# Optimization experiments

Hardware: AMD Instinct MI355X
Metric: run time of the kernel (lower is better)

The kernel has to match this reference:

```python
import jax, jax.numpy as jnp
import numpy as np

T, A, H, E = 16, 8, 128, 32  # steps, actions/step, hidden, embed


def setup_inputs() -> dict:
    key = jax.random.key(0)
    ks = jax.random.split(key, 16)
    n = lambda k, s: jax.random.normal(k, s, dtype=jnp.float32) * 0.1
    return {
        "old_actions": jax.random.randint(ks[0], (T,), 0, A),
        "init_input": n(ks[1], (1, E)),
        "W_ih_a": n(ks[2], (4 * H, E)), "W_hh_a": n(ks[3], (4 * H, H)),
        "b_ih_a": n(ks[4], (4 * H,)), "b_hh_a": n(ks[5], (4 * H,)),
        "heads_W": n(ks[6], (T, A, H)), "heads_b": n(ks[7], (T, A)),
        "W_ih_c": n(ks[8], (4 * H, E)), "W_hh_c": n(ks[9], (4 * H, H)),
        "b_ih_c": n(ks[10], (4 * H,)), "b_hh_c": n(ks[11], (4 * H,)),
        "critic_W": n(ks[12], (1, H)), "critic_b": n(ks[13], (1,)),
        "embed": n(ks[14], (T * A, E)),
    }


def _lstm_cell(x, h, c, W_ih, W_hh, b_ih, b_hh):
    # PyTorch LSTMCell: gate order i, f, g, o
    g = W_ih @ x + b_ih + W_hh @ h + b_hh
    i, f, gg, o = jnp.split(g, 4)
    c = jax.nn.sigmoid(f) * c + jax.nn.sigmoid(i) * jnp.tanh(gg)
    h = jax.nn.sigmoid(o) * jnp.tanh(c)
    return h, c


def reference(old_actions, init_input, W_ih_a, W_hh_a, b_ih_a, b_hh_a,
              heads_W, heads_b, W_ih_c, W_hh_c, b_ih_c, b_hh_c,
              critic_W, critic_b, embed):
    # input sequence is fully determined by the given actions
    global_idx = jnp.arange(T) * A + old_actions          # action offsets
    emb_rows = embed[global_idx]                          # [T, E]
    x_seq = jnp.concatenate([init_input, emb_rows[:-1]], axis=0)  # [T, E]

    def step(carry, xs):
        h_a, c_a, h_c, c_c = carry
        x, hw, hb, a = xs
        h_a, c_a = _lstm_cell(x, h_a, c_a, W_ih_a, W_hh_a, b_ih_a, b_hh_a)
        logits = hw @ h_a + hb                            # [A]
        logp = jax.nn.log_softmax(logits)
        probs = jnp.exp(logp)
        lp = logp[a]
        ent = -jnp.sum(probs * logp)
        h_c, c_c = _lstm_cell(x, h_c, c_c, W_ih_c, W_hh_c, b_ih_c, b_hh_c)
        val = critic_W[0] @ h_c + critic_b[0]
        return (h_a, c_a, h_c, c_c), (lp, ent, val)

    z = jnp.zeros((H,), jnp.float32)
    _, (log_probs, entropies, values) = jax.lax.scan(
        step, (z, z, z, z), (x_seq, heads_W, heads_b, old_actions))
    return log_probs, entropies, values  # each [T]
```

## Files before the change

### kernel.cpp

```cpp
#include <hip/hip_runtime.h>
#include <math.h>

#define T 16
#define A 8
#define H 128
#define E 32
#define G (4*H)

#define WS_WHH(L)   ((size_t)(L) * 131072u)
#define WS_ACCX(L)  (262144u + (size_t)(L) * 16384u)

typedef _Float16 h2t __attribute__((ext_vector_type(2)));
typedef _Float16 h8t __attribute__((ext_vector_type(8)));

__device__ __forceinline__ float sigmoidf_(float x) {
    return 1.0f / (1.0f + __expf(-x));
}
__device__ __forceinline__ float tanhf_(float x) {
    return 1.0f - 2.0f / (1.0f + __expf(2.0f * x));
}

#if __has_builtin(__builtin_amdgcn_fdot2)
#define DOT2(a, b, c) __builtin_amdgcn_fdot2((a), (b), (c), false)
#else
__device__ __forceinline__ float dot2_fb(h2t a, h2t b, float c) {
    return fmaf((float)a[0], (float)b[0], fmaf((float)a[1], (float)b[1], c));
}
#define DOT2(a, b, c) dot2_fb((a), (b), (c))
#endif

#define RPT16(M) M(0) M(1) M(2) M(3) M(4) M(5) M(6) M(7) \
                 M(8) M(9) M(10) M(11) M(12) M(13) M(14) M(15)

__global__ __launch_bounds__(256)
void ppo_prep_kernel(const int* __restrict__ old_actions,
                     const float* __restrict__ init_input,
                     const float* __restrict__ W_ih_a, const float* __restrict__ W_hh_a,
                     const float* __restrict__ b_ih_a, const float* __restrict__ b_hh_a,
                     const float* __restrict__ W_ih_c, const float* __restrict__ W_hh_c,
                     const float* __restrict__ b_ih_c, const float* __restrict__ b_hh_c,
                     const float* __restrict__ embed,
                     char* __restrict__ ws)
{
    const int b = blockIdx.x;
    if (b < 64) {
        int tau  = b * 256 + threadIdx.x;
        int lstm = tau >> 13;
        int i    = tau & 8191;
        int r    = i >> 4;
        int c    = i & 15;
        const float* W = (lstm == 0) ? W_hh_a : W_hh_c;
        const float* src = W + r * H + c * 8;
        float4 fa = *(const float4*)(src);
        float4 fb = *(const float4*)(src + 4);
        h8t p = { (_Float16)fa.x, (_Float16)fa.y, (_Float16)fa.z, (_Float16)fa.w,
                  (_Float16)fb.x, (_Float16)fb.y, (_Float16)fb.z, (_Float16)fb.w };
        *(h8t*)(ws + WS_WHH(lstm) + (size_t)(c * 512 + r) * 16u) = p;
    } else {
        int tau  = (b - 64) * 256 + threadIdx.x;
        int lstm = tau >> 13;
        int i    = tau & 8191;
        int t    = i >> 9;
        int r    = i & 511;
        const float* W_ih = (lstm == 0) ? W_ih_a : W_ih_c;
        const float* b_ih = (lstm == 0) ? b_ih_a : b_ih_c;
        const float* b_hh = (lstm == 0) ? b_hh_a : b_hh_c;
        const float* xp = (t == 0) ? init_input
                                   : embed + ((t - 1) * A + old_actions[t - 1]) * E;
        const float* wr = W_ih + r * E;
        float s0 = 0.f, s1 = 0.f, s2 = 0.f, s3 = 0.f;
        #pragma unroll
        for (int e = 0; e < E; e += 4) {
            float4 wv = *(const float4*)(wr + e);
            float4 xv = *(const float4*)(xp + e);
            s0 = fmaf(wv.x, xv.x, s0); s1 = fmaf(wv.y, xv.y, s1);
            s2 = fmaf(wv.z, xv.z, s2); s3 = fmaf(wv.w, xv.w, s3);
        }
        float acc = b_ih[r] + b_hh[r] + ((s0 + s1) + (s2 + s3));
        *(_Float16*)(ws + WS_ACCX(lstm) + (size_t)(t * 512 + r) * 2u) = (_Float16)acc;
    }
}

__global__ __attribute__((amdgpu_flat_work_group_size(512, 512),
                          amdgpu_waves_per_eu(2, 2)))
void ppo_ctrl_kernel(const int* __restrict__ old_actions,
                     const float* __restrict__ heads_W, const float* __restrict__ heads_b,
                     const float* __restrict__ critic_W, const float* __restrict__ critic_b,
                     const char* __restrict__ ws,
                     float* __restrict__ out)
{
    const int tid  = threadIdx.x;
    const int lane = tid & 63;
    const int wv   = tid >> 6;
    const int lstm = blockIdx.x;
    const bool actor = (lstm == 0);

    __shared__ __align__(16) float gates_s[G];
    __shared__ __align__(16) _Float16 h16[H];
    __shared__ __align__(16) _Float16 hhist[T][H];

    const char* wbase = ws + WS_WHH(lstm);
#define LOADW(i) h8t w##i = *(const h8t*)(wbase + (size_t)((i) * 512 + tid) * 16u); \
        asm volatile("" : "+v"(w##i));
    RPT16(LOADW)
#undef LOADW

    const _Float16* accg = (const _Float16*)(ws + WS_ACCX(lstm));

    float c_reg = 0.0f;
    const h8t* hv = (const h8t*)h16;

    #pragma unroll 1
    for (int t = 0; t < T; ++t) {
        float axv = (float)accg[t * 512 + tid];
        float a0 = 0.f, a1 = 0.f, a2 = 0.f, a3 = 0.f;
        if (t != 0) {
#define MACC(i) { h8t hq = hv[i];                                          \
            a0 = DOT2(__builtin_shufflevector(w##i, w##i, 0, 1),           \
                      __builtin_shufflevector(hq,  hq,  0, 1), a0);        \
            a1 = DOT2(__builtin_shufflevector(w##i, w##i, 2, 3),           \
                      __builtin_shufflevector(hq,  hq,  2, 3), a1);        \
            a2 = DOT2(__builtin_shufflevector(w##i, w##i, 4, 5),           \
                      __builtin_shufflevector(hq,  hq,  4, 5), a2);        \
            a3 = DOT2(__builtin_shufflevector(w##i, w##i, 6, 7),           \
                      __builtin_shufflevector(hq,  hq,  6, 7), a3); }
            RPT16(MACC)
#undef MACC
        }
        gates_s[tid] = axv + ((a0 + a1) + (a2 + a3));
        __syncthreads();

        if (tid < H) {
            float gi = gates_s[tid],       gf = gates_s[tid + H];
            float gg = gates_s[tid + 2*H], go = gates_s[tid + 3*H];
            float cn = sigmoidf_(gf) * c_reg + sigmoidf_(gi) * tanhf_(gg);
            c_reg = cn;
            float hvv = sigmoidf_(go) * tanhf_(cn);
            _Float16 hf = (_Float16)hvv;
            h16[tid] = hf;
            hhist[t][tid] = hf;
        }
        __syncthreads();
    }

    if (actor) {
        #pragma unroll
        for (int rep = 0; rep < 2; ++rep) {
            const int tt = wv + rep * 8;
            float hA = (float)hhist[tt][lane];
            float hB = (float)hhist[tt][64 + lane];
#define LOGIT(a) float l##a; {                                            \
            const float* hw = heads_W + (tt * A + (a)) * H;               \
            float p = fmaf(hw[lane], hA, hw[64 + lane] * hB);             \
            p += __shfl_xor(p, 1);  p += __shfl_xor(p, 2);                \
            p += __shfl_xor(p, 4);  p += __shfl_xor(p, 8);                \
            p += __shfl_xor(p, 16); p += __shfl_xor(p, 32);               \
            l##a = p + heads_b[tt * A + (a)]; }
            LOGIT(0) LOGIT(1) LOGIT(2) LOGIT(3)
            LOGIT(4) LOGIT(5) LOGIT(6) LOGIT(7)
#undef LOGIT
            if (lane == 0) {
                float m = fmaxf(fmaxf(fmaxf(l0, l1), fmaxf(l2, l3)),
                                fmaxf(fmaxf(l4, l5), fmaxf(l6, l7)));
                float e0 = __expf(l0 - m), e1 = __expf(l1 - m),
                      e2 = __expf(l2 - m), e3 = __expf(l3 - m),
                      e4 = __expf(l4 - m), e5 = __expf(l5 - m),
                      e6 = __expf(l6 - m), e7 = __expf(l7 - m);
                float s = ((e0 + e1) + (e2 + e3)) + ((e4 + e5) + (e6 + e7));
                float logZ = m + __logf(s);
                int act = old_actions[tt];
                float la = (act == 0) ? l0 : (act == 1) ? l1 : (act == 2) ? l2 :
                           (act == 3) ? l3 : (act == 4) ? l4 : (act == 5) ? l5 :
                           (act == 6) ? l6 : l7;
                out[tt] = la - logZ;
                float w_ = e0*(l0-logZ) + e1*(l1-logZ) + e2*(l2-logZ) + e3*(l3-logZ)
                         + e4*(l4-logZ) + e5*(l5-logZ) + e6*(l6-logZ) + e7*(l7-logZ);
                out[T + tt] = -w_ / s;
            }
        }
    } else {
        #pragma unroll
        for (int rep = 0; rep < 2; ++rep) {
            const int tt = wv + rep * 8;
            float hA = (float)hhist[tt][lane];
            float hB = (float)hhist[tt][64 + lane];
            float p = fmaf(critic_W[lane], hA, critic_W[64 + lane] * hB);
            p += __shfl_xor(p, 1);  p += __shfl_xor(p, 2);
            p += __shfl_xor(p, 4);  p += __shfl_xor(p, 8);
            p += __shfl_xor(p, 16); p += __shfl_xor(p, 32);
            if (lane == 0) out[2 * T + tt] = p + critic_b[0];
        }
    }
}

extern "C" void kernel_launch(void* const* d_in, const int* in_sizes, int n_in,
                              void* d_out, int out_size, void* d_ws, size_t ws_size,
                              hipStream_t stream) {
    const int*   old_actions = (const int*)  d_in[0];
    const float* init_input  = (const float*)d_in[1];
    const float* W_ih_a      = (const float*)d_in[2];
    const float* W_hh_a      = (const float*)d_in[3];
    const float* b_ih_a      = (const float*)d_in[4];
    const float* b_hh_a      = (const float*)d_in[5];
    const float* heads_W     = (const float*)d_in[6];
    const float* heads_b     = (const float*)d_in[7];
    const float* W_ih_c      = (const float*)d_in[8];
    const float* W_hh_c      = (const float*)d_in[9];
    const float* b_ih_c      = (const float*)d_in[10];
    const float* b_hh_c      = (const float*)d_in[11];
    const float* critic_W    = (const float*)d_in[12];
    const float* critic_b    = (const float*)d_in[13];
    const float* embed       = (const float*)d_in[14];
    float* out = (float*)d_out;
    char* ws = (char*)d_ws;

    ppo_prep_kernel<<<dim3(128), dim3(256), 0, stream>>>(
        old_actions, init_input,
        W_ih_a, W_hh_a, b_ih_a, b_hh_a,
        W_ih_c, W_hh_c, b_ih_c, b_hh_c,
        embed, ws);

    ppo_ctrl_kernel<<<dim3(2), dim3(512), 0, stream>>>(
        old_actions, heads_W, heads_b, critic_W, critic_b, ws, out);
}
```

Baseline: 27.90 us.

## Preload input-gate terms into LDS and hoist head weights before recurrence

```diff
diff --git a/kernel.cpp b/kernel.cpp
--- a/kernel.cpp
+++ b/kernel.cpp
@@ -8,7 +8,7 @@
 #define G (4*H)
 
 #define WS_WHH(L)   ((size_t)(L) * 131072u)
-#define WS_ACCX(L)  (262144u + (size_t)(L) * 16384u)
+#define WS_ACCX(L)  (262144u + (size_t)(L) * 32768u)
 
 typedef _Float16 h2t __attribute__((ext_vector_type(2)));
 typedef _Float16 h8t __attribute__((ext_vector_type(8)));
@@ -31,6 +31,7 @@
 
 #define RPT16(M) M(0) M(1) M(2) M(3) M(4) M(5) M(6) M(7) \
                  M(8) M(9) M(10) M(11) M(12) M(13) M(14) M(15)
+#define RPT8(M)  M(0) M(1) M(2) M(3) M(4) M(5) M(6) M(7)
 
 __global__ __launch_bounds__(256)
 void ppo_prep_kernel(const int* __restrict__ old_actions,
@@ -77,7 +78,7 @@
             s2 = fmaf(wv.z, xv.z, s2); s3 = fmaf(wv.w, xv.w, s3);
         }
         float acc = b_ih[r] + b_hh[r] + ((s0 + s1) + (s2 + s3));
-        *(_Float16*)(ws + WS_ACCX(lstm) + (size_t)(t * 512 + r) * 2u) = (_Float16)acc;
+        *(float*)(ws + WS_ACCX(lstm) + (size_t)(t * 512 + r) * 4u) = acc;
     }
 }
 
@@ -95,9 +96,16 @@
     const int lstm = blockIdx.x;
     const bool actor = (lstm == 0);
 
+    __shared__ __align__(16) float accx_lds[T * G];
     __shared__ __align__(16) float gates_s[G];
     __shared__ __align__(16) _Float16 h16[H];
     __shared__ __align__(16) _Float16 hhist[T][H];
+
+    const float4* asrc = (const float4*)(ws + WS_ACCX(lstm));
+    float4 ax0 = asrc[         tid];
+    float4 ax1 = asrc[ 512 +   tid];
+    float4 ax2 = asrc[1024 +   tid];
+    float4 ax3 = asrc[1536 +   tid];
 
     const char* wbase = ws + WS_WHH(lstm);
 #define LOADW(i) h8t w##i = *(const h8t*)(wbase + (size_t)((i) * 512 + tid) * 16u); \
@@ -105,14 +113,34 @@
     RPT16(LOADW)
 #undef LOADW
 
-    const _Float16* accg = (const _Float16*)(ws + WS_ACCX(lstm));
+    const int tt0 = wv, tt1 = wv + 8;
+#define HWLOAD(a) \
+    float hl0##a = heads_W[(tt0 * A + (a)) * H + lane]; \
+    float hh0##a = heads_W[(tt0 * A + (a)) * H + 64 + lane]; \
+    float hl1##a = heads_W[(tt1 * A + (a)) * H + lane]; \
+    float hh1##a = heads_W[(tt1 * A + (a)) * H + 64 + lane]; \
+    asm volatile("" : "+v"(hl0##a), "+v"(hh0##a), "+v"(hl1##a), "+v"(hh1##a));
+    RPT8(HWLOAD)
+#undef HWLOAD
+    float hbv0 = heads_b[tt0 * A + (lane & 7)];
+    float hbv1 = heads_b[tt1 * A + (lane & 7)];
+    float cw0 = critic_W[lane], cw1 = critic_W[64 + lane], cb = critic_b[0];
+    int act0 = old_actions[tt0], act1 = old_actions[tt1];
+    asm volatile("" : "+v"(hbv0), "+v"(hbv1), "+v"(cw0), "+v"(cw1), "+v"(cb));
+
+    float4* adst = (float4*)accx_lds;
+    adst[         tid] = ax0;
+    adst[ 512 +   tid] = ax1;
+    adst[1024 +   tid] = ax2;
+    adst[1536 +   tid] = ax3;
+    __syncthreads();
 
     float c_reg = 0.0f;
     const h8t* hv = (const h8t*)h16;
 
     #pragma unroll 1
     for (int t = 0; t < T; ++t) {
-        float axv = (float)accg[t * 512 + tid];
+        float axv = accx_lds[t * 512 + tid];
         float a0 = 0.f, a1 = 0.f, a2 = 0.f, a3 = 0.f;
         if (t != 0) {
 #define MACC(i) { h8t hq = hv[i];                                          \
@@ -144,51 +172,56 @@
     }
 
     if (actor) {
-        #pragma unroll
-        for (int rep = 0; rep < 2; ++rep) {
-            const int tt = wv + rep * 8;
-            float hA = (float)hhist[tt][lane];
-            float hB = (float)hhist[tt][64 + lane];
-#define LOGIT(a) float l##a; {                                            \
-            const float* hw = heads_W + (tt * A + (a)) * H;               \
-            float p = fmaf(hw[lane], hA, hw[64 + lane] * hB);             \
-            p += __shfl_xor(p, 1);  p += __shfl_xor(p, 2);                \
-            p += __shfl_xor(p, 4);  p += __shfl_xor(p, 8);                \
-            p += __shfl_xor(p, 16); p += __shfl_xor(p, 32);               \
-            l##a = p + heads_b[tt * A + (a)]; }
-            LOGIT(0) LOGIT(1) LOGIT(2) LOGIT(3)
-            LOGIT(4) LOGIT(5) LOGIT(6) LOGIT(7)
+#define HEADS(rep) {                                                      \
+        const int tt = tt##rep;                                           \
+        float hA = (float)hhist[tt][lane];                                \
+        float hB = (float)hhist[tt][64 + lane];                           \
+        float l0,l1,l2,l3,l4,l5,l6,l7;                                    \
+        {                                                                 \
+_Pragma("unroll")                                                         \
+        for (int dummy = 0; dummy < 1; ++dummy) {}                        \
+        }                                                                 \
+        LOGIT(rep,0,l0) LOGIT(rep,1,l1) LOGIT(rep,2,l2) LOGIT(rep,3,l3)   \
+        LOGIT(rep,4,l4) LOGIT(rep,5,l5) LOGIT(rep,6,l6) LOGIT(rep,7,l7)   \
+        if (lane == 0) {                                                  \
+            float m = fmaxf(fmaxf(fmaxf(l0, l1), fmaxf(l2, l3)),          \
+                            fmaxf(fmaxf(l4, l5), fmaxf(l6, l7)));         \
+            float e0 = __expf(l0 - m), e1 = __expf(l1 - m),               \
+                  e2 = __expf(l2 - m), e3 = __expf(l3 - m),               \
+                  e4 = __expf(l4 - m), e5 = __expf(l5 - m),               \
+                  e6 = __expf(l6 - m), e7 = __expf(l7 - m);               \
+            float s = ((e0 + e1) + (e2 + e3)) + ((e4 + e5) + (e6 + e7));  \
+            float logZ = m + __logf(s);                                   \
+            int act = act##rep;                                           \
+            float la = (act == 0) ? l0 : (act == 1) ? l1 : (act == 2) ? l2 : \
+                       (act == 3) ? l3 : (act == 4) ? l4 : (act == 5) ? l5 : \
+                       (act == 6) ? l6 : l7;                              \
+            out[tt] = la - logZ;                                          \
+            float w_ = e0*(l0-logZ) + e1*(l1-logZ) + e2*(l2-logZ) + e3*(l3-logZ) \
+                     + e4*(l4-logZ) + e5*(l5-logZ) + e6*(l6-logZ) + e7*(l7-logZ); \
+            out[T + tt] = -w_ / s;                                        \
+        } }
+#define LOGIT(rep,a,dst) {                                                \
+        float p = fmaf(hl##rep##a, hA, hh##rep##a * hB);                  \
+        p += __shfl_xor(p, 1);  p += __shfl_xor(p, 2);                    \
+        p += __shfl_xor(p, 4);  p += __shfl_xor(p, 8);                    \
+        p += __shfl_xor(p, 16); p += __shfl_xor(p, 32);                   \
+        dst = p + __shfl(hbv##rep, (a)); }
+        HEADS(0)
+        HEADS(1)
 #undef LOGIT
-            if (lane == 0) {
-                float m = fmaxf(fmaxf(fmaxf(l0, l1), fmaxf(l2, l3)),
-                                fmaxf(fmaxf(l4, l5), fmaxf(l6, l7)));
-                float e0 = __expf(l0 - m), e1 = __expf(l1 - m),
-                      e2 = __expf(l2 - m), e3 = __expf(l3 - m),
-                      e4 = __expf(l4 - m), e5 = __expf(l5 - m),
-                      e6 = __expf(l6 - m), e7 = __expf(l7 - m);
-                float s = ((e0 + e1) + (e2 + e3)) + ((e4 + e5) + (e6 + e7));
-                float logZ = m + __logf(s);
-                int act = old_actions[tt];
-                float la = (act == 0) ? l0 : (act == 1) ? l1 : (act == 2) ? l2 :
-                           (act == 3) ? l3 : (act == 4) ? l4 : (act == 5) ? l5 :
-                           (act == 6) ? l6 : l7;
-                out[tt] = la - logZ;
-                float w_ = e0*(l0-logZ) + e1*(l1-logZ) + e2*(l2-logZ) + e3*(l3-logZ)
-                         + e4*(l4-logZ) + e5*(l5-logZ) + e6*(l6-logZ) + e7*(l7-logZ);
-                out[T + tt] = -w_ / s;
-            }
-        }
+#undef HEADS
     } else {
         #pragma unroll
         for (int rep = 0; rep < 2; ++rep) {
-            const int tt = wv + rep * 8;
+            const int tt = (rep == 0) ? tt0 : tt1;
             float hA = (float)hhist[tt][lane];
             float hB = (float)hhist[tt][64 + lane];
-            float p = fmaf(critic_W[lane], hA, critic_W[64 + lane] * hB);
+            float p = fmaf(cw0, hA, cw1 * hB);
             p += __shfl_xor(p, 1);  p += __shfl_xor(p, 2);
             p += __shfl_xor(p, 4);  p += __shfl_xor(p, 8);
             p += __shfl_xor(p, 16); p += __shfl_xor(p, 32);
-            if (lane == 0) out[2 * T + tt] = p + critic_b[0];
+            if (lane == 0) out[2 * T + tt] = p + cb;
         }
     }
 }
```

Result: slower. 29.08 us (+4.2%).
